# Performance work log

Hardware: AMD Instinct MI355X
Metric: run time of the kernel (lower is better)

The kernel has to match this reference:

```python
import jax, jax.numpy as jnp
import numpy as np

N_NODES = 100000
N_EDGES = 1600000
D_IN = 128
D_HID = 128
D_OUT = 32


def setup_inputs() -> dict:
    key = jax.random.key(0)
    ks = jax.random.split(key, 10)
    x = jax.random.normal(ks[0], (N_NODES, D_IN), dtype=jnp.float32)
    edge_index = jax.random.randint(ks[1], (2, N_EDGES), 0, N_NODES, dtype=jnp.int64)
    s = 0.05
    return {
        "x": x,
        "edge_index": edge_index,
        "Wl0": jax.random.normal(ks[2], (D_IN, D_HID), jnp.float32) * s,
        "bl0": jnp.zeros((D_HID,), jnp.float32),
        "Wr0": jax.random.normal(ks[3], (D_IN, D_HID), jnp.float32) * s,
        "Wl1": jax.random.normal(ks[4], (D_HID, D_HID), jnp.float32) * s,
        "bl1": jnp.zeros((D_HID,), jnp.float32),
        "Wr1": jax.random.normal(ks[5], (D_HID, D_HID), jnp.float32) * s,
        "Wl2": jax.random.normal(ks[6], (D_HID, D_OUT), jnp.float32) * s,
        "bl2": jnp.zeros((D_OUT,), jnp.float32),
        "Wr2": jax.random.normal(ks[7], (D_HID, D_OUT), jnp.float32) * s,
    }


def _sage_conv(x, src, dst, Wl, bl, Wr):
    # PyG SAGEConv (aggr='mean', root_weight=True):
    # out[i] = lin_l(mean_{j in N(i)} x_j) + lin_r(x_i)
    n = x.shape[0]
    msgs = x[src]                                        # [E, F] gather
    agg = jax.ops.segment_sum(msgs, dst, num_segments=n) # [N, F] scatter-add
    deg = jax.ops.segment_sum(jnp.ones((src.shape[0],), x.dtype), dst, num_segments=n)
    mean = agg / jnp.maximum(deg, 1.0)[:, None]
    return mean @ Wl + bl + x @ Wr


def reference(x, edge_index, Wl0, bl0, Wr0, Wl1, bl1, Wr1, Wl2, bl2, Wr2):
    src, dst = edge_index[0], edge_index[1]
    h = jax.nn.relu(_sage_conv(x, src, dst, Wl0, bl0, Wr0))
    h = jax.nn.relu(_sage_conv(h, src, dst, Wl1, bl1, Wr1))
    h = _sage_conv(h, src, dst, Wl2, bl2, Wr2)
    return jax.nn.log_softmax(h, axis=1)
```

## Files before the change

### kernel.cpp

```cpp
#include <hip/hip_runtime.h>
#include <hip/hip_bf16.h>
#include <math.h>

#define NN 100000
#define NE 1600000

#define NCB 391
#define EB  8192
#define SCT 512
#define HBK 64
#define NSB 196
#define WPB 144

typedef __attribute__((ext_vector_type(8))) short short8;
typedef __attribute__((ext_vector_type(4))) float f32x4;

__device__ __forceinline__ unsigned short f2bf(float f) {
  union { float f; unsigned int i; } v; v.f = f;
  unsigned int i = v.i;
  unsigned int r = (i + 0x7FFFu + ((i >> 16) & 1u)) >> 16;
  return (unsigned short)r;
}
__device__ __forceinline__ float bflo(unsigned int u) {
  union { unsigned int i; float f; } v; v.i = u << 16; return v.f;
}
__device__ __forceinline__ float bfhi(unsigned int u) {
  union { unsigned int i; float f; } v; v.i = u & 0xFFFF0000u; return v.f;
}
__device__ __forceinline__ float bf1(unsigned short u) {
  union { unsigned int i; float f; } v; v.i = ((unsigned int)u) << 16; return v.f;
}

__global__ __launch_bounds__(512) void k_prep(
    const int* __restrict__ dst, int* __restrict__ part,
    const float* __restrict__ Wl0, const float* __restrict__ Wr0,
    const float* __restrict__ Wl1, const float* __restrict__ Wr1,
    const float* __restrict__ Wl2, const float* __restrict__ Wr2,
    unsigned short* __restrict__ B0, unsigned short* __restrict__ B1,
    unsigned short* __restrict__ B2) {
  if (blockIdx.x < HBK) {
    __shared__ int h[NCB];
    for (int i = threadIdx.x; i < NCB; i += 512) h[i] = 0;
    __syncthreads();
    int stride = HBK * 512;
    for (int e = blockIdx.x * 512 + threadIdx.x; e < NE; e += stride) {
      int d = dst[e];
      d = d < 0 ? 0 : (d >= NN ? NN - 1 : d);
      atomicAdd(&h[d >> 8], 1);
    }
    __syncthreads();
    for (int i = threadIdx.x; i < NCB; i += 512) part[blockIdx.x * NCB + i] = h[i];
  } else {
    int idx = (blockIdx.x - HBK) * 512 + threadIdx.x;
    if (idx < 32768) {
      int n = idx >> 7, k = idx & 127;
      float v = (n < 128) ? Wl0[k * 128 + n] : Wr0[k * 128 + (n - 128)];
      B0[idx] = f2bf(v);
    } else if (idx < 65536) {
      int j = idx - 32768;
      int n = j >> 7, k = j & 127;
      float v = (n < 128) ? Wl1[k * 128 + n] : Wr1[k * 128 + (n - 128)];
      B1[j] = f2bf(v);
    } else if (idx < 73728) {
      int j = idx - 65536;
      int n = j >> 7, k = j & 127;
      float v = (n < 32) ? Wl2[k * 32 + n] : Wr2[k * 32 + (n - 32)];
      B2[j] = f2bf(v);
    }
  }
}

__global__ __launch_bounds__(512) void k_cscan(const int* __restrict__ part,
                                               int* __restrict__ cboff,
                                               int* __restrict__ ccur,
                                               int* __restrict__ csroff) {
  __shared__ int sd[512];
  int t = threadIdx.x;
  int v = 0;
  if (t < NCB) {
    int s0 = 0, s1 = 0, s2 = 0, s3 = 0;
    #pragma unroll 4
    for (int k = 0; k < HBK; k += 4) {
      s0 += part[(k + 0) * NCB + t];
      s1 += part[(k + 1) * NCB + t];
      s2 += part[(k + 2) * NCB + t];
      s3 += part[(k + 3) * NCB + t];
    }
    v = (s0 + s1) + (s2 + s3);
    ccur[t] = 0;
  }
  sd[t] = v;
  __syncthreads();
  for (int st = 1; st < 512; st <<= 1) {
    int x = (t >= st) ? sd[t - st] : 0;
    __syncthreads();
    sd[t] += x;
    __syncthreads();
  }
  if (t < NCB) cboff[t] = sd[t] - v;
  if (t == NCB - 1) { cboff[NCB] = sd[t]; csroff[NN] = sd[t]; }
}


__device__ __forceinline__ void cscatter_body(
    char* smem, int bid,
    const int* __restrict__ src, const int* __restrict__ dst,
    const int* __restrict__ cboff, int* __restrict__ ccur,
    unsigned int* __restrict__ ebuf) {
  int* lh = (int*)smem;
  unsigned int* sRank = (unsigned int*)(smem + 1600);
  unsigned int* sPay  = (unsigned int*)(smem + 1600 + EB * 4);
  int t = threadIdx.x;
  int base = bid * EB;
  for (int i = t; i < NCB; i += SCT) lh[i] = 0;
  __syncthreads();
  #pragma unroll
  for (int i = 0; i < EB / SCT; i++) {
    int idx = i * SCT + t;
    int e = base + idx;
    unsigned int rk = 0xFFFFFFFFu, pv = 0;
    if (e < NE) {
      int d = dst[e];
      d = d < 0 ? 0 : (d >= NN ? NN - 1 : d);
      int s = src[e];
      s = s < 0 ? 0 : (s >= NN ? NN - 1 : s);
      int cb = d >> 8;
      int r = atomicAdd(&lh[cb], 1);
      rk = (((unsigned int)cb) << 13) | (unsigned int)r;
      pv = (((unsigned int)(d & 255)) << 17) | (unsigned int)s;
    }
    sRank[idx] = rk;
    sPay[idx]  = pv;
  }
  __syncthreads();
  for (int i = t; i < NCB; i += SCT) {
    int c = lh[i];
    int g = c ? atomicAdd(&ccur[i], c) : 0;
    lh[i] = cboff[i] + g;
  }
  __syncthreads();
  #pragma unroll
  for (int i = 0; i < EB / SCT; i++) {
    int idx = i * SCT + t;
    unsigned int rk = sRank[idx];
    if (rk != 0xFFFFFFFFu) {
      int cb = rk >> 13;
      int r  = rk & 0x1FFF;
      ebuf[lh[cb] + r] = sPay[idx];
    }
  }
}

__device__ __forceinline__ void mgemm0_body(
    char* smem, int bid, const float* __restrict__ A,
    const unsigned short* __restrict__ Bp, const float* __restrict__ bias,
    unsigned short* __restrict__ yl, unsigned short* __restrict__ yr) {
  unsigned short* sA = (unsigned short*)smem;
  int tid = threadIdx.x;
  int nb  = bid * 128;

  #pragma unroll
  for (int i = 0; i < 8; i++) {
    int j = i * 512 + tid;
    int m = j >> 5;
    int k4 = (j & 31) * 4;
    int gn = nb + m;
    float4 v = make_float4(0.f, 0.f, 0.f, 0.f);
    if (gn < NN) v = *(const float4*)&A[gn * 128 + k4];
    unsigned int p0 = (unsigned int)f2bf(v.x) | ((unsigned int)f2bf(v.y) << 16);
    unsigned int p1 = (unsigned int)f2bf(v.z) | ((unsigned int)f2bf(v.w) << 16);
    *(uint2*)&sA[m * 136 + k4] = make_uint2(p0, p1);
  }
  __syncthreads();

  int wave = tid >> 6, lane = tid & 63;
  int l15 = lane & 15, lq = lane >> 4;
  int wm = wave & 1, wn = wave >> 1;
  int mbase = wm * 64;
  int nbase = wn * 64;

  f32x4 acc[4][4];
  #pragma unroll
  for (int mi = 0; mi < 4; mi++)
    #pragma unroll
    for (int ni = 0; ni < 4; ni++) acc[mi][ni] = (f32x4){0.f, 0.f, 0.f, 0.f};

  #pragma unroll
  for (int kc = 0; kc < 4; kc++) {
    int k0 = kc * 32 + lq * 8;
    short8 af[4], bfr[4];
    #pragma unroll
    for (int ni = 0; ni < 4; ni++)
      bfr[ni] = *(const short8*)&Bp[(nbase + ni * 16 + l15) * 128 + k0];
    #pragma unroll
    for (int mi = 0; mi < 4; mi++)
      af[mi] = *(const short8*)&sA[(mbase + mi * 16 + l15) * 136 + k0];
    #pragma unroll
    for (int mi = 0; mi < 4; mi++)
      #pragma unroll
      for (int ni = 0; ni < 4; ni++)
        acc[mi][ni] = __builtin_amdgcn_mfma_f32_16x16x32_bf16(
            af[mi], bfr[ni], acc[mi][ni], 0, 0, 0);
  }

  #pragma unroll
  for (int mi = 0; mi < 4; mi++) {
    #pragma unroll
    for (int ni = 0; ni < 4; ni++) {
      int n = nbase + ni * 16 + l15;
      #pragma unroll
      for (int r = 0; r < 4; r++) {
        int gn = nb + mbase + mi * 16 + lq * 4 + r;
        if (gn < NN) {
          float v = acc[mi][ni][r];
          if (n < 128) {
            yl[(size_t)gn * 128 + n] = f2bf(v);
          } else {
            int n2 = n - 128;
            yr[(size_t)gn * 128 + n2] = f2bf(v + bias[n2]);
          }
        }
      }
    }
  }
}

__global__ __launch_bounds__(512) void k_scatgemm(
    const int* __restrict__ src, const int* __restrict__ dst,
    const int* __restrict__ cboff, int* __restrict__ ccur,
    unsigned int* __restrict__ ebuf,
    const float* __restrict__ x, const unsigned short* __restrict__ B0,
    const float* __restrict__ bias,
    unsigned short* __restrict__ yl, unsigned short* __restrict__ yr) {
  __shared__ char smem[1600 + EB * 8];
  if (blockIdx.x < NSB) {
    cscatter_body(smem, blockIdx.x, src, dst, cboff, ccur, ebuf);
  } else {
    mgemm0_body(smem, blockIdx.x - NSB, x, B0, bias, yl, yr);
  }
}

__global__ __launch_bounds__(256) void k_crefine(
    const unsigned int* __restrict__ ebuf, const int* __restrict__ cboff,
    int* __restrict__ csroff, float* __restrict__ invd,
    int* __restrict__ csrsrc) {
  __shared__ int lh[256], pos[256], cur[256];
  int b = blockIdx.x, t = threadIdx.x;
  lh[t] = 0; cur[t] = 0;
  __syncthreads();
  int beg = cboff[b], end = cboff[b + 1];
  for (int i = beg + t; i < end; i += 256) atomicAdd(&lh[ebuf[i] >> 17], 1);
  __syncthreads();
  int v = lh[t];
  pos[t] = v;
  __syncthreads();
  for (int st = 1; st < 256; st <<= 1) {
    int x = (t >= st) ? pos[t - st] : 0;
    __syncthreads();
    pos[t] += x;
    __syncthreads();
  }
  int nid = b * 256 + t;
  int mybase = cboff[b] + pos[t] - v;
  if (nid < NN) {
    csroff[nid] = mybase;
    invd[nid] = 1.0f / (float)(v < 1 ? 1 : v);
  }
  __syncthreads();
  pos[t] = mybase;
  __syncthreads();
  for (int i = beg + t; i < end; i += 256) {
    unsigned int u = ebuf[i];
    int local = u >> 17;
    int r = atomicAdd(&cur[local], 1);
    csrsrc[pos[local] + r] = (int)(u & 0x1FFFFu);
  }
}

template <int NC>
__global__ __launch_bounds__(512) void k_mgemm(
    const unsigned short* __restrict__ A, const unsigned short* __restrict__ Bp,
    const float* __restrict__ bias,
    unsigned short* __restrict__ yl, unsigned short* __restrict__ yr) {
  __shared__ unsigned short sA[128 * 136];
  int tid = threadIdx.x;
  int nb  = blockIdx.x * 128;

  #pragma unroll
  for (int i = 0; i < 4; i++) {
    int j = i * 512 + tid;
    int m = j >> 4;
    int k8 = (j & 15) * 8;
    int gn = nb + m;
    uint4 v = make_uint4(0, 0, 0, 0);
    if (gn < NN) v = *(const uint4*)&A[gn * 128 + k8];
    *(uint4*)&sA[m * 136 + k8] = v;
  }
  __syncthreads();

  int wave = tid >> 6, lane = tid & 63;
  int l15 = lane & 15, lq = lane >> 4;
  constexpr int MT = (NC == 256) ? 4 : 2;
  constexpr int NT = (NC == 256) ? 4 : 2;
  int wm, wn;
  if (NC == 256) { wm = wave & 1; wn = wave >> 1; }
  else           { wm = wave >> 1; wn = wave & 1; }
  int mbase = wm * (MT * 16);
  int nbase = wn * (NT * 16);

  f32x4 acc[MT][NT];
  #pragma unroll
  for (int mi = 0; mi < MT; mi++)
    #pragma unroll
    for (int ni = 0; ni < NT; ni++) acc[mi][ni] = (f32x4){0.f, 0.f, 0.f, 0.f};

  #pragma unroll
  for (int kc = 0; kc < 4; kc++) {
    int k0 = kc * 32 + lq * 8;
    short8 af[MT], bfr[NT];
    #pragma unroll
    for (int ni = 0; ni < NT; ni++)
      bfr[ni] = *(const short8*)&Bp[(nbase + ni * 16 + l15) * 128 + k0];
    #pragma unroll
    for (int mi = 0; mi < MT; mi++)
      af[mi] = *(const short8*)&sA[(mbase + mi * 16 + l15) * 136 + k0];
    #pragma unroll
    for (int mi = 0; mi < MT; mi++)
      #pragma unroll
      for (int ni = 0; ni < NT; ni++)
        acc[mi][ni] = __builtin_amdgcn_mfma_f32_16x16x32_bf16(
            af[mi], bfr[ni], acc[mi][ni], 0, 0, 0);
  }

  constexpr int HC = NC / 2;
  #pragma unroll
  for (int mi = 0; mi < MT; mi++) {
    #pragma unroll
    for (int ni = 0; ni < NT; ni++) {
      int n = nbase + ni * 16 + l15;
      #pragma unroll
      for (int r = 0; r < 4; r++) {
        int gn = nb + mbase + mi * 16 + lq * 4 + r;
        if (gn < NN) {
          float v = acc[mi][ni][r];
          if (n < HC) {
            yl[(size_t)gn * HC + n] = f2bf(v);
          } else {
            int n2 = n - HC;
            yr[(size_t)gn * HC + n2] = f2bf(v + bias[n2]);
          }
        }
      }
    }
  }
}

#define ACC8(u) do { \
  a0 += bflo((u).x); a1 += bfhi((u).x); \
  a2 += bflo((u).y); a3 += bfhi((u).y); \
  a4 += bflo((u).z); a5 += bfhi((u).z); \
  a6 += bflo((u).w); a7 += bfhi((u).w); } while (0)

__global__ __launch_bounds__(256) void k_agg128(
    const unsigned short* __restrict__ yl, const unsigned short* __restrict__ yr,
    const int* __restrict__ off, const int* __restrict__ csr,
    const float* __restrict__ invd, unsigned short* __restrict__ out, int relu) {
  int wid  = (blockIdx.x * 256 + threadIdx.x) >> 6;
  int lane = threadIdx.x & 63;
  if (wid >= NN) return;
  int beg = off[wid], end = off[wid + 1];
  int deg = end - beg;
  int q   = lane >> 4;
  int l16 = lane & 15;
  const uint4* ylp = (const uint4*)yl;

  float sc = invd[wid];
  uint4 rv = ((const uint4*)yr)[wid * 16 + l16];

  float a0 = 0.f, a1 = 0.f, a2 = 0.f, a3 = 0.f;
  float a4 = 0.f, a5 = 0.f, a6 = 0.f, a7 = 0.f;

  for (int w0 = 0; w0 < deg; w0 += 64) {
    int ei = w0 + lane;
    int sv = (ei < deg) ? csr[beg + ei] : 0;
    int wcnt = deg - w0; if (wcnt > 64) wcnt = 64;
    int full = wcnt >> 2;
    int p = 0;
    for (; p + 4 <= full; p += 4) {
      int b = p * 4 + q;
      int s0 = __shfl(sv, b,      64);
      int s1 = __shfl(sv, b + 4,  64);
      int s2 = __shfl(sv, b + 8,  64);
      int s3 = __shfl(sv, b + 12, 64);
      uint4 u0 = ylp[s0 * 16 + l16];
      uint4 u1 = ylp[s1 * 16 + l16];
      uint4 u2 = ylp[s2 * 16 + l16];
      uint4 u3 = ylp[s3 * 16 + l16];
      ACC8(u0); ACC8(u1); ACC8(u2); ACC8(u3);
    }
    for (; p < full; p++) {
      int s0 = __shfl(sv, p * 4 + q, 64);
      uint4 u0 = ylp[s0 * 16 + l16];
      ACC8(u0);
    }
    int rem = wcnt & 3;
    if (rem && q < rem) {
      int s0 = __shfl(sv, full * 4 + q, 64);
      uint4 u0 = ylp[s0 * 16 + l16];
      ACC8(u0);
    }
  }

  a0 += __shfl_xor(a0, 16, 64); a0 += __shfl_xor(a0, 32, 64);
  a1 += __shfl_xor(a1, 16, 64); a1 += __shfl_xor(a1, 32, 64);
  a2 += __shfl_xor(a2, 16, 64); a2 += __shfl_xor(a2, 32, 64);
  a3 += __shfl_xor(a3, 16, 64); a3 += __shfl_xor(a3, 32, 64);
  a4 += __shfl_xor(a4, 16, 64); a4 += __shfl_xor(a4, 32, 64);
  a5 += __shfl_xor(a5, 16, 64); a5 += __shfl_xor(a5, 32, 64);
  a6 += __shfl_xor(a6, 16, 64); a6 += __shfl_xor(a6, 32, 64);
  a7 += __shfl_xor(a7, 16, 64); a7 += __shfl_xor(a7, 32, 64);

  float v0 = a0 * sc + bflo(rv.x), v1 = a1 * sc + bfhi(rv.x);
  float v2 = a2 * sc + bflo(rv.y), v3 = a3 * sc + bfhi(rv.y);
  float v4 = a4 * sc + bflo(rv.z), v5 = a5 * sc + bfhi(rv.z);
  float v6 = a6 * sc + bflo(rv.w), v7 = a7 * sc + bfhi(rv.w);
  if (relu) {
    v0 = fmaxf(v0, 0.f); v1 = fmaxf(v1, 0.f);
    v2 = fmaxf(v2, 0.f); v3 = fmaxf(v3, 0.f);
    v4 = fmaxf(v4, 0.f); v5 = fmaxf(v5, 0.f);
    v6 = fmaxf(v6, 0.f); v7 = fmaxf(v7, 0.f);
  }
  if (q == 0) {
    unsigned int p0 = (unsigned int)f2bf(v0) | ((unsigned int)f2bf(v1) << 16);
    unsigned int p1 = (unsigned int)f2bf(v2) | ((unsigned int)f2bf(v3) << 16);
    unsigned int p2 = (unsigned int)f2bf(v4) | ((unsigned int)f2bf(v5) << 16);
    unsigned int p3 = (unsigned int)f2bf(v6) | ((unsigned int)f2bf(v7) << 16);
    ((uint4*)out)[wid * 16 + l16] = make_uint4(p0, p1, p2, p3);
  }
}

#define ACC4(u) do { \
  a0 += bflo((u).x); a1 += bfhi((u).x); \
  a2 += bflo((u).y); a3 += bfhi((u).y); } while (0)

__global__ __launch_bounds__(256) void k_agg32_lsm(
    const unsigned short* __restrict__ yl, const unsigned short* __restrict__ yr,
    const int* __restrict__ off, const int* __restrict__ csr,
    const float* __restrict__ invd, float* __restrict__ out) {
  int wid  = (blockIdx.x * 256 + threadIdx.x) >> 6;
  int lane = threadIdx.x & 63;
  if (wid >= NN) return;
  int beg = off[wid], end = off[wid + 1];
  int deg = end - beg;
  int q  = lane >> 3;
  int l8 = lane & 7;
  const uint2* ylp = (const uint2*)yl;

  float sc = invd[wid];
  uint2 rv = ((const uint2*)yr)[wid * 8 + l8];

  float a0 = 0.f, a1 = 0.f, a2 = 0.f, a3 = 0.f;

  for (int w0 = 0; w0 < deg; w0 += 64) {
    int ei = w0 + lane;
    int sv = (ei < deg) ? csr[beg + ei] : 0;
    int wcnt = deg - w0; if (wcnt > 64) wcnt = 64;
    int full = wcnt >> 3;
    int p = 0;
    for (; p + 2 <= full; p += 2) {
      int b = p * 8 + q;
      int s0 = __shfl(sv, b,     64);
      int s1 = __shfl(sv, b + 8, 64);
      uint2 u0 = ylp[s0 * 8 + l8];
      uint2 u1 = ylp[s1 * 8 + l8];
      ACC4(u0); ACC4(u1);
    }
    for (; p < full; p++) {
      int s0 = __shfl(sv, p * 8 + q, 64);
      uint2 u0 = ylp[s0 * 8 + l8];
      ACC4(u0);
    }
    int rem = wcnt & 7;
    if (rem && q < rem) {
      int s0 = __shfl(sv, full * 8 + q, 64);
      uint2 u0 = ylp[s0 * 8 + l8];
      ACC4(u0);
    }
  }

  a0 += __shfl_xor(a0, 8, 64); a0 += __shfl_xor(a0, 16, 64); a0 += __shfl_xor(a0, 32, 64);
  a1 += __shfl_xor(a1, 8, 64); a1 += __shfl_xor(a1, 16, 64); a1 += __shfl_xor(a1, 32, 64);
  a2 += __shfl_xor(a2, 8, 64); a2 += __shfl_xor(a2, 16, 64); a2 += __shfl_xor(a2, 32, 64);
  a3 += __shfl_xor(a3, 8, 64); a3 += __shfl_xor(a3, 16, 64); a3 += __shfl_xor(a3, 32, 64);

  float v0 = a0 * sc + bflo(rv.x), v1 = a1 * sc + bfhi(rv.x);
  float v2 = a2 * sc + bflo(rv.y), v3 = a3 * sc + bfhi(rv.y);

  float m = fmaxf(fmaxf(v0, v1), fmaxf(v2, v3));
  m = fmaxf(m, __shfl_xor(m, 1, 64));
  m = fmaxf(m, __shfl_xor(m, 2, 64));
  m = fmaxf(m, __shfl_xor(m, 4, 64));
  float e0 = expf(v0 - m), e1 = expf(v1 - m);
  float e2 = expf(v2 - m), e3 = expf(v3 - m);
  float s = (e0 + e1) + (e2 + e3);
  s += __shfl_xor(s, 1, 64);
  s += __shfl_xor(s, 2, 64);
  s += __shfl_xor(s, 4, 64);
  float ls = logf(s);
  if (q == 0) {
    float4 o = make_float4(v0 - m - ls, v1 - m - ls, v2 - m - ls, v3 - m - ls);
    ((float4*)out)[wid * 8 + l8] = o;
  }
}


extern "C" void kernel_launch(void* const* d_in, const int* in_sizes, int n_in,
                              void* d_out, int out_size, void* d_ws, size_t ws_size,
                              hipStream_t stream) {
  (void)in_sizes; (void)n_in; (void)out_size; (void)ws_size;
  const float* x   = (const float*)d_in[0];
  const int*   ei  = (const int*)d_in[1];
  const float* Wl0 = (const float*)d_in[2];
  const float* bl0 = (const float*)d_in[3];
  const float* Wr0 = (const float*)d_in[4];
  const float* Wl1 = (const float*)d_in[5];
  const float* bl1 = (const float*)d_in[6];
  const float* Wr1 = (const float*)d_in[7];
  const float* Wl2 = (const float*)d_in[8];
  const float* bl2 = (const float*)d_in[9];
  const float* Wr2 = (const float*)d_in[10];
  const int* srcI = ei;
  const int* dstI = ei + NE;

  char* w = (char*)d_ws;
  int*   ccur   = (int*)(w + (16 << 10));
  int*   cboff  = (int*)(w + (32 << 10));
  unsigned short* B0 = (unsigned short*)(w + (64 << 10));
  unsigned short* B1 = (unsigned short*)(w + (160 << 10));
  unsigned short* B2 = (unsigned short*)(w + (256 << 10));
  int*   part   = (int*)(w + (288 << 10));
  int*   csroff = (int*)(w + (512 << 10));
  float* invd   = (float*)(w + (1024 << 10));
  unsigned int* ebuf = (unsigned int*)(w + (size_t)(2) * 1024 * 1024);
  int*   csrsrc = (int*)(w + (size_t)(9) * 1024 * 1024);
  unsigned short* ylb = (unsigned short*)(w + (size_t)(16) * 1024 * 1024);
  unsigned short* yrb = (unsigned short*)(w + (size_t)(48) * 1024 * 1024);
  unsigned short* hb  = (unsigned short*)(w + (size_t)(80) * 1024 * 1024);

  dim3 gg((NN + 127) / 128);

  k_prep<<<HBK + WPB, 512, 0, stream>>>(dstI, part, Wl0, Wr0, Wl1, Wr1, Wl2, Wr2,
                                        B0, B1, B2);
  k_cscan<<<1, 512, 0, stream>>>(part, cboff, ccur, csroff);
  k_scatgemm<<<NSB + 782, 512, 0, stream>>>(srcI, dstI, cboff, ccur, ebuf,
                                            x, B0, bl0, ylb, yrb);
  k_crefine<<<NCB, 256, 0, stream>>>(ebuf, cboff, csroff, invd, csrsrc);
  k_agg128<<<(NN * 64) / 256, 256, 0, stream>>>(ylb, yrb, csroff, csrsrc, invd, hb, 1);
  k_mgemm<256><<<gg, 512, 0, stream>>>(hb, B1, bl1, ylb, yrb);
  k_agg128<<<(NN * 64) / 256, 256, 0, stream>>>(ylb, yrb, csroff, csrsrc, invd, hb, 1);
  k_mgemm<64><<<gg, 512, 0, stream>>>(hb, B2, bl2, ylb, yrb);
  k_agg32_lsm<<<(NN * 64) / 256, 256, 0, stream>>>(ylb, yrb, csroff, csrsrc, invd,
                                                   (float*)d_out);
}
```

Before: 416.7 us.

## Keep scatter ranks in registers, halve edges per block, pad global counters

```diff
diff --git a/kernel.cpp b/kernel.cpp
--- a/kernel.cpp
+++ b/kernel.cpp
@@ -6,10 +6,11 @@
 #define NE 1600000
 
 #define NCB 391
-#define EB  8192
+#define EB  4096
 #define SCT 512
+#define EPT 8
 #define HBK 64
-#define NSB 196
+#define NSB 391
 #define WPB 144
 
 typedef __attribute__((ext_vector_type(8))) short short8;
@@ -87,7 +88,7 @@
       s3 += part[(k + 3) * NCB + t];
     }
     v = (s0 + s1) + (s2 + s3);
-    ccur[t] = 0;
+    ccur[t * 16] = 0;
   }
   sd[t] = v;
   __syncthreads();
@@ -108,17 +109,16 @@
     const int* __restrict__ cboff, int* __restrict__ ccur,
     unsigned int* __restrict__ ebuf) {
   int* lh = (int*)smem;
-  unsigned int* sRank = (unsigned int*)(smem + 1600);
-  unsigned int* sPay  = (unsigned int*)(smem + 1600 + EB * 4);
   int t = threadIdx.x;
   int base = bid * EB;
   for (int i = t; i < NCB; i += SCT) lh[i] = 0;
   __syncthreads();
-  #pragma unroll
-  for (int i = 0; i < EB / SCT; i++) {
-    int idx = i * SCT + t;
-    int e = base + idx;
-    unsigned int rk = 0xFFFFFFFFu, pv = 0;
+  unsigned int rk[EPT], pv[EPT];
+  #pragma unroll
+  for (int i = 0; i < EPT; i++) {
+    int e = base + i * SCT + t;
+    rk[i] = 0xFFFFFFFFu;
+    pv[i] = 0;
     if (e < NE) {
       int d = dst[e];
       d = d < 0 ? 0 : (d >= NN ? NN - 1 : d);
@@ -126,27 +126,22 @@
       s = s < 0 ? 0 : (s >= NN ? NN - 1 : s);
       int cb = d >> 8;
       int r = atomicAdd(&lh[cb], 1);
-      rk = (((unsigned int)cb) << 13) | (unsigned int)r;
-      pv = (((unsigned int)(d & 255)) << 17) | (unsigned int)s;
-    }
-    sRank[idx] = rk;
-    sPay[idx]  = pv;
+      rk[i] = (((unsigned int)cb) << 13) | (unsigned int)r;
+      pv[i] = (((unsigned int)(d & 255)) << 17) | (unsigned int)s;
+    }
   }
   __syncthreads();
   for (int i = t; i < NCB; i += SCT) {
     int c = lh[i];
-    int g = c ? atomicAdd(&ccur[i], c) : 0;
+    int g = c ? atomicAdd(&ccur[i * 16], c) : 0;
     lh[i] = cboff[i] + g;
   }
   __syncthreads();
   #pragma unroll
-  for (int i = 0; i < EB / SCT; i++) {
-    int idx = i * SCT + t;
-    unsigned int rk = sRank[idx];
-    if (rk != 0xFFFFFFFFu) {
-      int cb = rk >> 13;
-      int r  = rk & 0x1FFF;
-      ebuf[lh[cb] + r] = sPay[idx];
+  for (int i = 0; i < EPT; i++) {
+    unsigned int r = rk[i];
+    if (r != 0xFFFFFFFFu) {
+      ebuf[lh[r >> 13] + (r & 0x1FFF)] = pv[i];
     }
   }
 }
@@ -225,14 +220,14 @@
   }
 }
 
-__global__ __launch_bounds__(512) void k_scatgemm(
+__global__ __launch_bounds__(512, 4) void k_scatgemm(
     const int* __restrict__ src, const int* __restrict__ dst,
     const int* __restrict__ cboff, int* __restrict__ ccur,
     unsigned int* __restrict__ ebuf,
     const float* __restrict__ x, const unsigned short* __restrict__ B0,
     const float* __restrict__ bias,
     unsigned short* __restrict__ yl, unsigned short* __restrict__ yr) {
-  __shared__ char smem[1600 + EB * 8];
+  __shared__ char smem[128 * 136 * 2];
   if (blockIdx.x < NSB) {
     cscatter_body(smem, blockIdx.x, src, dst, cboff, ccur, ebuf);
   } else {
@@ -533,12 +528,12 @@
   const int* dstI = ei + NE;
 
   char* w = (char*)d_ws;
-  int*   ccur   = (int*)(w + (16 << 10));
   int*   cboff  = (int*)(w + (32 << 10));
   unsigned short* B0 = (unsigned short*)(w + (64 << 10));
   unsigned short* B1 = (unsigned short*)(w + (160 << 10));
   unsigned short* B2 = (unsigned short*)(w + (256 << 10));
   int*   part   = (int*)(w + (288 << 10));
+  int*   ccur   = (int*)(w + (416 << 10));
   int*   csroff = (int*)(w + (512 << 10));
   float* invd   = (float*)(w + (1024 << 10));
   unsigned int* ebuf = (unsigned int*)(w + (size_t)(2) * 1024 * 1024);
```

Result: no change. 417.5 us (+0.2%).
